# Kernel optimization log

Measured on AMD Instinct MI355X. Metric: run time of the kernel, lower is better.

Reference implementation:

```python
import jax, jax.numpy as jnp
import numpy as np
from jax import lax

B, C, H, W = 4, 4, 64, 64
NREF = 16
DECAY = 0.8
MAX_DELAY = 24
WET_MIX, FEEDBACK, ROOM = 0.3, 0.4, 0.5  # module defaults (static Python floats)
HEADS = 4  # min(4, channels)


def _conv2d(x, w, b, pad, groups=1):
    y = lax.conv_general_dilated(x, w, (1, 1), [(pad, pad), (pad, pad)],
                                 dimension_numbers=('NCHW', 'OIHW', 'NCHW'),
                                 feature_group_count=groups)
    return y if b is None else y + b[None, :, None, None]


def _fade(n, fw=4):
    f = np.ones(n, np.float32)
    f[:fw] = np.linspace(0.6, 1.0, fw)
    f[-fw:] = np.linspace(1.0, 0.6, fw)
    return jnp.asarray(f)


def _delay_line(x, delay, yf, xf):
    # torch: shifts=(int(delay*1), int(delay*2)) on dims (2,3); delay>0 so int==floor
    ys = jnp.floor(delay).astype(jnp.int32)
    xs = jnp.floor(delay * 2.0).astype(jnp.int32)
    s = jnp.roll(x, shift=(ys, xs), axis=(2, 3))
    # shifts are always nonzero here (scaled delays >= 6), so both fades apply
    return s * yf[None, None, :, None] * xf[None, None, None, :]


def setup_inputs() -> dict:
    key = jax.random.key(0)
    ks = jax.random.split(key, 16)
    n = jax.random.normal
    return {
        'x': n(ks[0], (B, C, H, W), jnp.float32),
        'reflection_weights': n(ks[1], (NREF,), jnp.float32) * 0.1,
        'reflection_delays': jax.random.randint(ks[2], (NREF,), 1, MAX_DELAY).astype(jnp.float32),
        'diffusion_strength': n(ks[3], (NREF,), jnp.float32) * 0.2,
        'spatial_w': n(ks[4], (2 * C, C, 3, 3), jnp.float32) * 0.1,
        'spatial_b': jnp.zeros((2 * C,), jnp.float32),
        'feedback_w': n(ks[5], (C, C, 3, 3), jnp.float32) * 0.1,
        'feedback_b': jnp.zeros((C,), jnp.float32),
        'damp1_w': n(ks[6], (C // 2, C, 1, 1), jnp.float32) * 0.3,
        'damp1_b': jnp.zeros((C // 2,), jnp.float32),
        'damp2_w': n(ks[7], (C, C // 2, 1, 1), jnp.float32) * 0.3,
        'damp2_b': jnp.zeros((C,), jnp.float32),
        'attn_in_w': n(ks[8], (3 * C, C), jnp.float32) * 0.3,
        'attn_in_b': jnp.zeros((3 * C,), jnp.float32),
        'attn_out_w': n(ks[9], (C, C), jnp.float32) * 0.3,
        'attn_out_b': jnp.zeros((C,), jnp.float32),
        'out_w': n(ks[10], (C, 3 * C, 1, 1), jnp.float32) * 0.2,
        'out_b': jnp.zeros((C,), jnp.float32),
    }


def reference(x, reflection_weights, reflection_delays, diffusion_strength,
              spatial_w, spatial_b, feedback_w, feedback_b,
              damp1_w, damp1_b, damp2_w, damp2_b,
              attn_in_w, attn_in_b, attn_out_w, attn_out_b, out_w, out_b):
    b, c, h, w = x.shape
    rsf = 8.0 / NREF  # reflection_scale_factor = 0.5
    scaled_delays = reflection_delays * ROOM * 12.0 * rsf
    wet = jnp.zeros_like(x)
    fb = x * 0.1
    spatial_features = _conv2d(x, spatial_w, spatial_b, 1)
    yf, xf = _fade(h), _fade(w)
    feedback_scale = 1.0 + rsf * 0.5
    for i in range(NREF):
        delay = scaled_delays[i]
        weight = jax.nn.sigmoid(reflection_weights[i]) * (DECAY ** i) * (1.0 + FEEDBACK * feedback_scale)
        r = _delay_line(fb, delay, yf, xf)
        r = _conv2d(r, feedback_w, feedback_b, 1)
        damping = jax.nn.sigmoid(
            _conv2d(jax.nn.silu(_conv2d(r, damp1_w, damp1_b, 0)), damp2_w, damp2_b, 0))
        r = r * damping
        wet = wet + r * weight * (4.0 * rsf)
        fb = fb + r * (FEEDBACK * 1.2 * rsf)
        if FEEDBACK > 0.3 and i > 0:
            prev = _delay_line(fb, delay * 0.5, yf, xf)
            fb = fb + prev * (FEEDBACK * 0.4 * rsf)
    # spatial self-attention over flattened pixels (embed=4, 4 heads, head_dim=1)
    S = h * w
    hd = c // HEADS
    wf = wet.reshape(b, c, S).transpose(0, 2, 1)  # [b, S, c]
    qkv = wf @ attn_in_w.T + attn_in_b
    q, k, v = jnp.split(qkv, 3, axis=-1)
    def split_heads(t):
        return t.reshape(b, S, HEADS, hd).transpose(0, 2, 1, 3)  # [b, H, S, hd]
    q, k, v = split_heads(q), split_heads(k), split_heads(v)
    scores = jnp.einsum('bhqd,bhkd->bhqk', q, k) / jnp.sqrt(jnp.float32(hd))
    attn = jax.nn.softmax(scores, axis=-1)
    o = jnp.einsum('bhqk,bhkd->bhqd', attn, v).transpose(0, 2, 1, 3).reshape(b, S, c)
    o = o @ attn_out_w.T + attn_out_b
    wet = o.transpose(0, 2, 1).reshape(b, c, h, w)
    # ROOM=0.5 > 0.3 -> box blur, kernel = max(3, int(0.5*3*0.5)) = 3
    kb = 3
    blur_k = jnp.ones((c, 1, kb, kb), jnp.float32) / (kb * kb)
    wet = _conv2d(wet, blur_k, None, kb // 2, groups=c)
    # FEEDBACK=0.4 > 0.2 -> edge enhancement
    ek = jnp.array([[-1., -1., -1.], [-1., 8., -1.], [-1., -1., -1.]], jnp.float32)
    edge_k = jnp.tile(ek[None, None], (c, 1, 1, 1))
    edge = _conv2d(wet, edge_k, None, 1, groups=c)
    wet = wet + edge * (FEEDBACK * 0.2 * rsf)
    # ROOM=0.5 <= 0.8 -> no contrast adjustment
    combined = jnp.concatenate([spatial_features, wet], axis=1)
    processed = _conv2d(combined, out_w, out_b, 0)
    return x * (1.0 - WET_MIX) + processed * WET_MIX
```

## Files before the change

### kernel.cpp

```cpp
#include <hip/hip_runtime.h>

#define LOG2E 1.4426950408889634f
#define RNB 32

typedef float v2f __attribute__((ext_vector_type(2)));

__device__ __forceinline__ float fsig(float z) {
    return __builtin_amdgcn_rcpf(1.0f + exp2f(-z * LOG2E));
}

__device__ __forceinline__ float4 ld_fb(const unsigned long long* p) {
    unsigned long long a = __hip_atomic_load(p,     __ATOMIC_RELAXED, __HIP_MEMORY_SCOPE_AGENT);
    unsigned long long b = __hip_atomic_load(p + 1, __ATOMIC_RELAXED, __HIP_MEMORY_SCOPE_AGENT);
    float2 lo = __builtin_bit_cast(float2, a);
    float2 hi = __builtin_bit_cast(float2, b);
    return make_float4(lo.x, lo.y, hi.x, hi.y);
}

__device__ __forceinline__ void st_fb(unsigned long long* p, float4 v) {
    __hip_atomic_store(p,     __builtin_bit_cast(unsigned long long, make_float2(v.x, v.y)),
                       __ATOMIC_RELAXED, __HIP_MEMORY_SCOPE_AGENT);
    __hip_atomic_store(p + 1, __builtin_bit_cast(unsigned long long, make_float2(v.z, v.w)),
                       __ATOMIC_RELAXED, __HIP_MEMORY_SCOPE_AGENT);
}

__global__ __launch_bounds__(256) void bar_init(unsigned* cnt) {
    for (int j = threadIdx.x; j < 1024; j += 256) cnt[j] = 0u;
}

__device__ __forceinline__ void conv_damp_l(
    const float4* __restrict__ src, int yq, int xq, int ys, int xs,
    const float* fe, const float4 wr[9][4],
    const float4 d1w0, const float4 d1w1, const float2 d1b, const float4 d2p[4],
    float rv[4])
{
    float r[4] = { d2p[0].w, d2p[1].w, d2p[2].w, d2p[3].w };
    #pragma unroll
    for (int a = 0; a < 3; ++a) {
        int yy = yq - 1 + a;
        float fy = fe[yy + 1];
        const float4* rowp = src + (((yy - ys) & 63) << 6);
        #pragma unroll
        for (int qq = 0; qq < 3; ++qq) {
            int xt = xq - 1 + qq;
            float f = fy * fe[xt + 1];
            float4 v = rowp[(xt - xs) & 63];
            float s0 = v.x * f, s1 = v.y * f, s2 = v.z * f, s3 = v.w * f;
            #pragma unroll
            for (int co = 0; co < 4; ++co) {
                float4 w = wr[a * 3 + qq][co];
                r[co] = fmaf(w.x, s0, fmaf(w.y, s1, fmaf(w.z, s2, fmaf(w.w, s3, r[co]))));
            }
        }
    }
    float z0 = fmaf(d1w0.x, r[0], fmaf(d1w0.y, r[1], fmaf(d1w0.z, r[2], fmaf(d1w0.w, r[3], d1b.x))));
    float z1 = fmaf(d1w1.x, r[0], fmaf(d1w1.y, r[1], fmaf(d1w1.z, r[2], fmaf(d1w1.w, r[3], d1b.y))));
    float h0 = z0 * fsig(z0);
    float h1 = z1 * fsig(z1);
    #pragma unroll
    for (int c = 0; c < 4; ++c) {
        float dm = fsig(fmaf(d2p[c].x, h0, fmaf(d2p[c].y, h1, d2p[c].z)));
        rv[c] = r[c] * dm;
    }
}

__global__ __launch_bounds__(512) void reverb_mb(
    const float* __restrict__ x, const float* __restrict__ rw, const float* __restrict__ dl,
    const float* __restrict__ fbw, const float* __restrict__ fbb,
    const float* __restrict__ d1wg, const float* __restrict__ d1bg,
    const float* __restrict__ d2wg, const float* __restrict__ d2bg,
    unsigned long long* __restrict__ GA, unsigned long long* __restrict__ GB,
    unsigned* __restrict__ cnt, float4* __restrict__ ws_wet)
{
    __shared__ float4 fbL[4096];
    __shared__ float fe[66];
    __shared__ float4 wvsL[36];
    __shared__ float s_rw[16], s_dl[16];
    __shared__ float4 s_mlp[7];

    const int tid = threadIdx.x;
    const int b   = blockIdx.x >> 3;
    const int blk = blockIdx.x & 7;

    if (tid < 66) {
        float f = 0.0f;
        if (tid >= 1 && tid <= 64) {
            int j = tid - 1;
            f = 1.0f;
            if (j < 4) f = 0.6f + (0.4f / 3.0f) * j;
            else if (j >= 60) f = 0.6f + (0.4f / 3.0f) * (63 - j);
        }
        fe[tid] = f;
    }
    if (tid >= 128 && tid < 164) {
        int t2 = tid - 128, n = t2 >> 2, co = t2 & 3;
        wvsL[t2] = make_float4(fbw[(co * 4 + 0) * 9 + n], fbw[(co * 4 + 1) * 9 + n],
                               fbw[(co * 4 + 2) * 9 + n], fbw[(co * 4 + 3) * 9 + n]);
    }
    if (tid >= 192 && tid < 208) s_rw[tid - 192] = rw[tid - 192];
    if (tid >= 256 && tid < 272) s_dl[tid - 256] = dl[tid - 256];
    if (tid == 320) {
        s_mlp[0] = make_float4(d1wg[0], d1wg[1], d1wg[2], d1wg[3]);
        s_mlp[1] = make_float4(d1wg[4], d1wg[5], d1wg[6], d1wg[7]);
        s_mlp[2] = make_float4(d1bg[0], d1bg[1], 0.0f, 0.0f);
        for (int c = 0; c < 4; ++c)
            s_mlp[3 + c] = make_float4(d2wg[c * 2], d2wg[c * 2 + 1], d2bg[c], fbb[c]);
    }
    for (int s = tid; s < 4096; s += 512) {
        float4 v;
        v.x = 0.1f * x[((b * 4 + 0) << 12) + s];
        v.y = 0.1f * x[((b * 4 + 1) << 12) + s];
        v.z = 0.1f * x[((b * 4 + 2) << 12) + s];
        v.w = 0.1f * x[((b * 4 + 3) << 12) + s];
        fbL[s] = v;
    }
    __syncthreads();

    float4 wr[9][4];
    #pragma unroll
    for (int n = 0; n < 9; ++n)
        #pragma unroll
        for (int co = 0; co < 4; ++co) wr[n][co] = wvsL[n * 4 + co];
    const float4 d1w0 = s_mlp[0], d1w1 = s_mlp[1];
    const float2 d1b = make_float2(s_mlp[2].x, s_mlp[2].y);
    float4 d2p[4] = { s_mlp[3], s_mlp[4], s_mlp[5], s_mlp[6] };

    const int ly = tid >> 6;
    const int y0 = (blk << 3) + ly;
    const int xx = tid & 63;
    float4 fbv = fbL[(y0 << 6) + xx];

    unsigned long long* Ab = GA + (b << 13);
    unsigned long long* Bb = GB + (b << 13);
    unsigned* cb = cnt + b * 240;

    float acc0 = 0.0f, acc1 = 0.0f, acc2 = 0.0f, acc3 = 0.0f;
    float decay = 1.0f;
    #pragma unroll 1
    for (int i = 0; i < 16; ++i) {
        float d = s_dl[i];
        int ys  = ((int)(3.0f * d)) & 63;
        int xs  = ((int)(6.0f * d)) & 63;
        float wgt = fsig(s_rw[i]) * decay * 3.0f;

        float rv[4];
        conv_damp_l(fbL, y0, xx, ys, xs, fe, wr, d1w0, d1w1, d1b, d2p, rv);
        acc0 = fmaf(rv[0], wgt, acc0);
        acc1 = fmaf(rv[1], wgt, acc1);
        acc2 = fmaf(rv[2], wgt, acc2);
        acc3 = fmaf(rv[3], wgt, acc3);
        float4 g = make_float4(fbv.x + 0.24f * rv[0], fbv.y + 0.24f * rv[1],
                               fbv.z + 0.24f * rv[2], fbv.w + 0.24f * rv[3]);
        if (i == 15) break;

        unsigned long long* G = (i & 1) ? Bb : Ab;
        st_fb(G + (((y0 << 6) + xx) << 1), g);

        __syncthreads();
        if (tid == 0)
            __hip_atomic_fetch_add(&cb[i * 16], 1u, __ATOMIC_RELAXED,
                                   __HIP_MEMORY_SCOPE_AGENT);
        if ((tid & 63) == 0) {
            while (__hip_atomic_load(&cb[i * 16], __ATOMIC_RELAXED,
                                     __HIP_MEMORY_SCOPE_AGENT) < 8u)
                __builtin_amdgcn_s_sleep(1);
        }
        asm volatile("" ::: "memory");

        int ys2 = ((int)(1.5f * d)) & 63;
        int xs2 = ((int)(3.0f * d)) & 63;
        float dn = s_dl[i + 1];
        int ysn = ((int)(3.0f * dn)) & 63;

        if (i > 0) {
            int yr = (y0 - ys2) & 63, xr = (xx - xs2) & 63;
            float4 g2 = ld_fb(G + (((yr << 6) + xr) << 1));
            float f = 0.08f * fe[y0 + 1] * fe[xx + 1];
            fbv = make_float4(fmaf(f, g2.x, g.x), fmaf(f, g2.y, g.y),
                              fmaf(f, g2.z, g.z), fmaf(f, g2.w, g.w));
        } else {
            fbv = g;
        }

        #pragma unroll
        for (int rpt = 0; rpt < 2; ++rpt) {
            int idx = tid + (rpt << 9);
            if (idx < 640) {
                int j  = idx >> 6, xc = idx & 63;
                int rr = ((blk << 3) - 1 + j - ysn) & 63;
                float4 g1 = ld_fb(G + (((rr << 6) + xc) << 1));
                float4 nv = g1;
                if (i > 0) {
                    int r2 = (rr - ys2) & 63, x2 = (xc - xs2) & 63;
                    float4 g2 = ld_fb(G + (((r2 << 6) + x2) << 1));
                    float f = 0.08f * fe[rr + 1] * fe[xc + 1];
                    nv = make_float4(fmaf(f, g2.x, g1.x), fmaf(f, g2.y, g1.y),
                                     fmaf(f, g2.z, g1.z), fmaf(f, g2.w, g1.w));
                }
                fbL[(rr << 6) + xc] = nv;
            }
        }
        __syncthreads();
        decay *= 0.8f;
    }

    ws_wet[(b << 12) + (y0 << 6) + xx] = make_float4(acc0, acc1, acc2, acc3);
}

__global__ __launch_bounds__(512) void attn_kernel(
    const float4* __restrict__ wet, const float* __restrict__ aiw,
    const float* __restrict__ aib, float* __restrict__ o_out)
{
    __shared__ float ksf[4096];
    __shared__ float vsf[4096];
    __shared__ float redmx[8], redmn[8];
    __shared__ float2 part[2048];

    const int tid = threadIdx.x;
    const int bid = blockIdx.x;
    const int b  = bid >> 7;
    const int h  = (bid >> 5) & 3;
    const int qc = bid & 31;

    float wq[4], wk[4], wv[4];
    #pragma unroll
    for (int c = 0; c < 4; ++c) {
        wq[c] = aiw[h * 4 + c];
        wk[c] = aiw[(4 + h) * 4 + c];
        wv[c] = aiw[(8 + h) * 4 + c];
    }
    const float bq = aib[h], bk = aib[4 + h], bv = aib[8 + h];

    float lmax = -1e30f, lmin = 1e30f;
    for (int s = tid; s < 4096; s += 512) {
        float4 w4 = wet[(b << 12) + s];
        float k = wk[0] * w4.x + wk[1] * w4.y + wk[2] * w4.z + wk[3] * w4.w + bk;
        float v = wv[0] * w4.x + wv[1] * w4.y + wv[2] * w4.z + wv[3] * w4.w + bv;
        ksf[s] = k; vsf[s] = v;
        lmax = fmaxf(lmax, k); lmin = fminf(lmin, k);
    }
    #pragma unroll
    for (int off = 32; off > 0; off >>= 1) {
        lmax = fmaxf(lmax, __shfl_xor(lmax, off));
        lmin = fminf(lmin, __shfl_xor(lmin, off));
    }
    if ((tid & 63) == 0) { redmx[tid >> 6] = lmax; redmn[tid >> 6] = lmin; }
    __syncthreads();
    float kmax = redmx[0], kmin = redmn[0];
    #pragma unroll
    for (int w = 1; w < 8; ++w) { kmax = fmaxf(kmax, redmx[w]); kmin = fminf(kmin, redmn[w]); }

    const int rs = tid & 31;
    const int kg = tid >> 5;
    v2f qL2[4], nmL2[4];
    #pragma unroll
    for (int rr = 0; rr < 4; ++rr) {
        int row = (qc << 7) + (rs << 2) + rr;
        float4 w4 = wet[(b << 12) + row];
        float q = wq[0] * w4.x + wq[1] * w4.y + wq[2] * w4.z + wq[3] * w4.w + bq;
        float m = (q >= 0.0f) ? q * kmax : q * kmin;
        float qL = q * LOG2E, mL = m * LOG2E;
        qL2[rr] = (v2f){qL, qL}; nmL2[rr] = (v2f){-mL, -mL};
    }

    const v2f* ks2 = (const v2f*)ksf;
    const v2f* vs2 = (const v2f*)vsf;
    v2f den2[4], num2[4];
    #pragma unroll
    for (int rr = 0; rr < 4; ++rr) { den2[rr] = (v2f){0.f, 0.f}; num2[rr] = (v2f){0.f, 0.f}; }

    const int j0 = kg << 6;
    #pragma unroll 4
    for (int j = j0 * 2; j < j0 * 2 + 128; ++j) {
        v2f kk = ks2[j];
        v2f vv = vs2[j];
        #pragma unroll
        for (int rr = 0; rr < 4; ++rr) {
            v2f arg = __builtin_elementwise_fma(qL2[rr], kk, nmL2[rr]);
            v2f e;
            e.x = __builtin_amdgcn_exp2f(arg.x);
            e.y = __builtin_amdgcn_exp2f(arg.y);
            den2[rr] += e;
            num2[rr] = __builtin_elementwise_fma(e, vv, num2[rr]);
        }
    }
    #pragma unroll
    for (int rr = 0; rr < 4; ++rr)
        part[(kg << 7) + (rs << 2) + rr] =
            make_float2(den2[rr].x + den2[rr].y, num2[rr].x + num2[rr].y);
    __syncthreads();
    if (tid < 128) {
        float dd = 0.0f, nn = 0.0f;
        #pragma unroll
        for (int g = 0; g < 16; ++g) {
            float2 p = part[(g << 7) + tid];
            dd += p.x; nn += p.y;
        }
        int row = (qc << 7) + tid;
        o_out[((b << 12) + row) * 4 + h] = nn * __builtin_amdgcn_rcpf(dd);
    }
}

__global__ __launch_bounds__(256) void tail_kernel(
    const float4* __restrict__ o_in, const float* __restrict__ aow,
    const float* __restrict__ aob, const float* __restrict__ x,
    const float* __restrict__ sw, const float* __restrict__ sb,
    const float* __restrict__ ow, const float* __restrict__ ob,
    float* __restrict__ out)
{
    __shared__ float wetp[4][8][64];
    __shared__ float blurL[4][6][64];
    __shared__ float xL[4][6][64];
    __shared__ float s_sw[288], s_ow[48], s_sb[8], s_ob[4];

    const int tid  = threadIdx.x;
    const int b    = blockIdx.x >> 4;
    const int band = blockIdx.x & 15;
    const int y0   = band << 2;

    float pw[4][4], pb[4];
    #pragma unroll
    for (int c = 0; c < 4; ++c) {
        #pragma unroll
        for (int h = 0; h < 4; ++h) pw[c][h] = aow[c * 4 + h];
        pb[c] = aob[c];
    }

    for (int j = tid; j < 288; j += 256) s_sw[j] = sw[j];
    if (tid < 48) s_ow[tid] = ow[tid];
    if (tid < 8)  s_sb[tid] = sb[tid];
    if (tid < 4)  s_ob[tid] = ob[tid];

    for (int s = tid; s < 512; s += 256) {
        int lr = s >> 6, xx = s & 63;
        int gy = y0 - 2 + lr;
        float4 o = make_float4(0.f, 0.f, 0.f, 0.f);
        if (gy >= 0 && gy < 64) o = o_in[(b << 12) + (gy << 6) + xx];
        #pragma unroll
        for (int c = 0; c < 4; ++c)
            wetp[c][lr][xx] = (gy >= 0 && gy < 64)
                ? pw[c][0]*o.x + pw[c][1]*o.y + pw[c][2]*o.z + pw[c][3]*o.w + pb[c]
                : 0.0f;
    }
    for (int s = tid; s < 1536; s += 256) {
        int c = s / 384, rm = s - c * 384;
        int r = rm >> 6, xx = rm & 63;
        int gy = y0 - 1 + r;
        float v = 0.f;
        if (gy >= 0 && gy < 64) v = x[((b * 4 + c) << 12) + (gy << 6) + xx];
        xL[c][r][xx] = v;
    }
    __syncthreads();

    for (int s = tid; s < 1536; s += 256) {
        int c = s / 384, rm = s - c * 384;
        int r = rm >> 6, xx = rm & 63;
        int gy = y0 - 1 + r;
        float acc = 0.f;
        if (gy >= 0 && gy < 64) {
            #pragma unroll
            for (int dy = 0; dy < 3; ++dy) {
                #pragma unroll
                for (int dx = -1; dx <= 1; ++dx) {
                    int xc = xx + dx;
                    if (xc >= 0 && xc <= 63) acc += wetp[c][r + dy][xc];
                }
            }
        }
        blurL[c][r][xx] = acc * (1.0f / 9.0f);
    }
    __syncthreads();

    {
        const int lyq = tid >> 6, xx = tid & 63;
        const int gy = y0 + lyq;

        float spat[8];
        #pragma unroll
        for (int co = 0; co < 8; ++co) spat[co] = s_sb[co];
        #pragma unroll
        for (int dy = 0; dy < 3; ++dy) {
            #pragma unroll
            for (int dx = -1; dx <= 1; ++dx) {
                int xc = xx + dx;
                if (xc < 0 || xc > 63) continue;
                int kx = dx + 1;
                #pragma unroll
                for (int ci = 0; ci < 4; ++ci) {
                    float xv = xL[ci][lyq + dy][xc];
                    #pragma unroll
                    for (int co = 0; co < 8; ++co)
                        spat[co] += s_sw[((co * 4 + ci) * 3 + dy) * 3 + kx] * xv;
                }
            }
        }

        float wetF[4];
        #pragma unroll
        for (int c = 0; c < 4; ++c) {
            float center = blurL[c][lyq + 1][xx];
            float sum9 = 0.f;
            #pragma unroll
            for (int dy = 0; dy < 3; ++dy) {
                #pragma unroll
                for (int dx = -1; dx <= 1; ++dx) {
                    int xc = xx + dx;
                    if (xc >= 0 && xc <= 63) sum9 += blurL[c][lyq + dy][xc];
                }
            }
            wetF[c] = center + 0.04f * (9.0f * center - sum9);
        }

        #pragma unroll
        for (int co = 0; co < 4; ++co) {
            float p = s_ob[co];
            #pragma unroll
            for (int j = 0; j < 8; ++j) p += s_ow[co * 12 + j] * spat[j];
            #pragma unroll
            for (int c = 0; c < 4; ++c) p += s_ow[co * 12 + 8 + c] * wetF[c];
            float xc = xL[co][lyq + 1][xx];
            out[((b * 4 + co) << 12) + (gy << 6) + xx] = 0.7f * xc + 0.3f * p;
        }
    }
}

extern "C" void kernel_launch(void* const* d_in, const int* in_sizes, int n_in,
                              void* d_out, int out_size, void* d_ws, size_t ws_size,
                              hipStream_t stream)
{
    (void)in_sizes; (void)n_in; (void)out_size; (void)ws_size;
    const float* x    = (const float*)d_in[0];
    const float* rw   = (const float*)d_in[1];
    const float* dl   = (const float*)d_in[2];
    const float* sw   = (const float*)d_in[4];
    const float* sb   = (const float*)d_in[5];
    const float* fbw  = (const float*)d_in[6];
    const float* fbb  = (const float*)d_in[7];
    const float* d1w  = (const float*)d_in[8];
    const float* d1b  = (const float*)d_in[9];
    const float* d2w  = (const float*)d_in[10];
    const float* d2b  = (const float*)d_in[11];
    const float* aiw  = (const float*)d_in[12];
    const float* aib  = (const float*)d_in[13];
    const float* aow  = (const float*)d_in[14];
    const float* aob  = (const float*)d_in[15];
    const float* ow   = (const float*)d_in[16];
    const float* ob   = (const float*)d_in[17];
    float* out = (float*)d_out;

    float* ws_wet  = (float*)d_ws;
    float* GA      = ws_wet + 65536;
    float* GB      = GA + 65536;
    unsigned* cnt  = (unsigned*)(GB + 65536);
    float* ws_o    = GA;

    bar_init<<<1, 256, 0, stream>>>(cnt);
    reverb_mb<<<RNB, 512, 0, stream>>>(x, rw, dl, fbw, fbb, d1w, d1b, d2w, d2b,
                                       (unsigned long long*)GA, (unsigned long long*)GB,
                                       cnt, (float4*)ws_wet);
    attn_kernel<<<512, 512, 0, stream>>>((const float4*)ws_wet, aiw, aib, ws_o);
    tail_kernel<<<64, 256, 0, stream>>>((const float4*)ws_o, aow, aob, x,
                                        sw, sb, ow, ob, out);
}
```

Baseline: 184.4 us.

## Fuse reverb and attention kernels with per-batch completion flags

```diff
diff --git a/kernel.cpp b/kernel.cpp
--- a/kernel.cpp
+++ b/kernel.cpp
@@ -64,240 +64,264 @@
     }
 }
 
-__global__ __launch_bounds__(512) void reverb_mb(
+struct SmemReverb {
+    float4 fbL[4096];
+    float  fe[66];
+    float4 wvsL[36];
+    float  s_rw[16], s_dl[16];
+    float4 s_mlp[7];
+};
+struct SmemAttn {
+    float  ksf[4096];
+    float  vsf[4096];
+    float  redmx[8], redmn[8];
+    float2 part[2048];
+};
+union SmemU { SmemReverb r; SmemAttn a; };
+
+__global__ __launch_bounds__(512) void fused_ra(
     const float* __restrict__ x, const float* __restrict__ rw, const float* __restrict__ dl,
     const float* __restrict__ fbw, const float* __restrict__ fbb,
     const float* __restrict__ d1wg, const float* __restrict__ d1bg,
     const float* __restrict__ d2wg, const float* __restrict__ d2bg,
     unsigned long long* __restrict__ GA, unsigned long long* __restrict__ GB,
-    unsigned* __restrict__ cnt, float4* __restrict__ ws_wet)
+    unsigned* __restrict__ cnt, unsigned long long* __restrict__ ws_wet,
+    const float* __restrict__ aiw, const float* __restrict__ aib,
+    float* __restrict__ o_out)
 {
-    __shared__ float4 fbL[4096];
-    __shared__ float fe[66];
-    __shared__ float4 wvsL[36];
-    __shared__ float s_rw[16], s_dl[16];
-    __shared__ float4 s_mlp[7];
-
+    __shared__ SmemU sm;
     const int tid = threadIdx.x;
-    const int b   = blockIdx.x >> 3;
-    const int blk = blockIdx.x & 7;
-
-    if (tid < 66) {
-        float f = 0.0f;
-        if (tid >= 1 && tid <= 64) {
-            int j = tid - 1;
-            f = 1.0f;
-            if (j < 4) f = 0.6f + (0.4f / 3.0f) * j;
-            else if (j >= 60) f = 0.6f + (0.4f / 3.0f) * (63 - j);
-        }
-        fe[tid] = f;
-    }
-    if (tid >= 128 && tid < 164) {
-        int t2 = tid - 128, n = t2 >> 2, co = t2 & 3;
-        wvsL[t2] = make_float4(fbw[(co * 4 + 0) * 9 + n], fbw[(co * 4 + 1) * 9 + n],
-                               fbw[(co * 4 + 2) * 9 + n], fbw[(co * 4 + 3) * 9 + n]);
-    }
-    if (tid >= 192 && tid < 208) s_rw[tid - 192] = rw[tid - 192];
-    if (tid >= 256 && tid < 272) s_dl[tid - 256] = dl[tid - 256];
-    if (tid == 320) {
-        s_mlp[0] = make_float4(d1wg[0], d1wg[1], d1wg[2], d1wg[3]);
-        s_mlp[1] = make_float4(d1wg[4], d1wg[5], d1wg[6], d1wg[7]);
-        s_mlp[2] = make_float4(d1bg[0], d1bg[1], 0.0f, 0.0f);
-        for (int c = 0; c < 4; ++c)
-            s_mlp[3 + c] = make_float4(d2wg[c * 2], d2wg[c * 2 + 1], d2bg[c], fbb[c]);
-    }
-    for (int s = tid; s < 4096; s += 512) {
-        float4 v;
-        v.x = 0.1f * x[((b * 4 + 0) << 12) + s];
-        v.y = 0.1f * x[((b * 4 + 1) << 12) + s];
-        v.z = 0.1f * x[((b * 4 + 2) << 12) + s];
-        v.w = 0.1f * x[((b * 4 + 3) << 12) + s];
-        fbL[s] = v;
-    }
-    __syncthreads();
-
-    float4 wr[9][4];
-    #pragma unroll
-    for (int n = 0; n < 9; ++n)
-        #pragma unroll
-        for (int co = 0; co < 4; ++co) wr[n][co] = wvsL[n * 4 + co];
-    const float4 d1w0 = s_mlp[0], d1w1 = s_mlp[1];
-    const float2 d1b = make_float2(s_mlp[2].x, s_mlp[2].y);
-    float4 d2p[4] = { s_mlp[3], s_mlp[4], s_mlp[5], s_mlp[6] };
-
-    const int ly = tid >> 6;
-    const int y0 = (blk << 3) + ly;
-    const int xx = tid & 63;
-    float4 fbv = fbL[(y0 << 6) + xx];
-
-    unsigned long long* Ab = GA + (b << 13);
-    unsigned long long* Bb = GB + (b << 13);
-    unsigned* cb = cnt + b * 240;
-
-    float acc0 = 0.0f, acc1 = 0.0f, acc2 = 0.0f, acc3 = 0.0f;
-    float decay = 1.0f;
-    #pragma unroll 1
-    for (int i = 0; i < 16; ++i) {
-        float d = s_dl[i];
-        int ys  = ((int)(3.0f * d)) & 63;
-        int xs  = ((int)(6.0f * d)) & 63;
-        float wgt = fsig(s_rw[i]) * decay * 3.0f;
-
-        float rv[4];
-        conv_damp_l(fbL, y0, xx, ys, xs, fe, wr, d1w0, d1w1, d1b, d2p, rv);
-        acc0 = fmaf(rv[0], wgt, acc0);
-        acc1 = fmaf(rv[1], wgt, acc1);
-        acc2 = fmaf(rv[2], wgt, acc2);
-        acc3 = fmaf(rv[3], wgt, acc3);
-        float4 g = make_float4(fbv.x + 0.24f * rv[0], fbv.y + 0.24f * rv[1],
-                               fbv.z + 0.24f * rv[2], fbv.w + 0.24f * rv[3]);
-        if (i == 15) break;
-
-        unsigned long long* G = (i & 1) ? Bb : Ab;
-        st_fb(G + (((y0 << 6) + xx) << 1), g);
-
+    const int bid = blockIdx.x;
+
+    if (bid < RNB) {
+        float4* fbL = sm.r.fbL;
+        float*  fe  = sm.r.fe;
+
+        const int b   = bid >> 3;
+        const int blk = bid & 7;
+
+        if (tid < 66) {
+            float f = 0.0f;
+            if (tid >= 1 && tid <= 64) {
+                int j = tid - 1;
+                f = 1.0f;
+                if (j < 4) f = 0.6f + (0.4f / 3.0f) * j;
+                else if (j >= 60) f = 0.6f + (0.4f / 3.0f) * (63 - j);
+            }
+            fe[tid] = f;
+        }
+        if (tid >= 128 && tid < 164) {
+            int t2 = tid - 128, n = t2 >> 2, co = t2 & 3;
+            sm.r.wvsL[t2] = make_float4(fbw[(co * 4 + 0) * 9 + n], fbw[(co * 4 + 1) * 9 + n],
+                                        fbw[(co * 4 + 2) * 9 + n], fbw[(co * 4 + 3) * 9 + n]);
+        }
+        if (tid >= 192 && tid < 208) sm.r.s_rw[tid - 192] = rw[tid - 192];
+        if (tid >= 256 && tid < 272) sm.r.s_dl[tid - 256] = dl[tid - 256];
+        if (tid == 320) {
+            sm.r.s_mlp[0] = make_float4(d1wg[0], d1wg[1], d1wg[2], d1wg[3]);
+            sm.r.s_mlp[1] = make_float4(d1wg[4], d1wg[5], d1wg[6], d1wg[7]);
+            sm.r.s_mlp[2] = make_float4(d1bg[0], d1bg[1], 0.0f, 0.0f);
+            for (int c = 0; c < 4; ++c)
+                sm.r.s_mlp[3 + c] = make_float4(d2wg[c * 2], d2wg[c * 2 + 1], d2bg[c], fbb[c]);
+        }
+        for (int s = tid; s < 4096; s += 512) {
+            float4 v;
+            v.x = 0.1f * x[((b * 4 + 0) << 12) + s];
+            v.y = 0.1f * x[((b * 4 + 1) << 12) + s];
+            v.z = 0.1f * x[((b * 4 + 2) << 12) + s];
+            v.w = 0.1f * x[((b * 4 + 3) << 12) + s];
+            fbL[s] = v;
+        }
+        __syncthreads();
+
+        float4 wr[9][4];
+        #pragma unroll
+        for (int n = 0; n < 9; ++n)
+            #pragma unroll
+            for (int co = 0; co < 4; ++co) wr[n][co] = sm.r.wvsL[n * 4 + co];
+        const float4 d1w0 = sm.r.s_mlp[0], d1w1 = sm.r.s_mlp[1];
+        const float2 d1b = make_float2(sm.r.s_mlp[2].x, sm.r.s_mlp[2].y);
+        float4 d2p[4] = { sm.r.s_mlp[3], sm.r.s_mlp[4], sm.r.s_mlp[5], sm.r.s_mlp[6] };
+
+        const int ly = tid >> 6;
+        const int y0 = (blk << 3) + ly;
+        const int xx = tid & 63;
+        float4 fbv = fbL[(y0 << 6) + xx];
+
+        unsigned long long* Ab = GA + (b << 13);
+        unsigned long long* Bb = GB + (b << 13);
+        unsigned* cb = cnt + b * 240;
+
+        float acc0 = 0.0f, acc1 = 0.0f, acc2 = 0.0f, acc3 = 0.0f;
+        float decay = 1.0f;
+        #pragma unroll 1
+        for (int i = 0; i < 16; ++i) {
+            float d = sm.r.s_dl[i];
+            int ys  = ((int)(3.0f * d)) & 63;
+            int xs  = ((int)(6.0f * d)) & 63;
+            float wgt = fsig(sm.r.s_rw[i]) * decay * 3.0f;
+
+            float rv[4];
+            conv_damp_l(fbL, y0, xx, ys, xs, fe, wr, d1w0, d1w1, d1b, d2p, rv);
+            acc0 = fmaf(rv[0], wgt, acc0);
+            acc1 = fmaf(rv[1], wgt, acc1);
+            acc2 = fmaf(rv[2], wgt, acc2);
+            acc3 = fmaf(rv[3], wgt, acc3);
+            float4 g = make_float4(fbv.x + 0.24f * rv[0], fbv.y + 0.24f * rv[1],
+                                   fbv.z + 0.24f * rv[2], fbv.w + 0.24f * rv[3]);
+            if (i == 15) break;
+
+            unsigned long long* G = (i & 1) ? Bb : Ab;
+            st_fb(G + (((y0 << 6) + xx) << 1), g);
+
+            __syncthreads();
+            if (tid == 0) {
+                if (__hip_atomic_fetch_add(&cb[i * 16], 1u, __ATOMIC_RELAXED,
+                                           __HIP_MEMORY_SCOPE_AGENT) + 1u < 8u) {
+                    while (__hip_atomic_load(&cb[i * 16], __ATOMIC_RELAXED,
+                                             __HIP_MEMORY_SCOPE_AGENT) < 8u)
+                        __builtin_amdgcn_s_sleep(1);
+                }
+            }
+            __syncthreads();
+
+            int ys2 = ((int)(1.5f * d)) & 63;
+            int xs2 = ((int)(3.0f * d)) & 63;
+            float dn = sm.r.s_dl[i + 1];
+            int ysn = ((int)(3.0f * dn)) & 63;
+
+            if (i > 0) {
+                int yr = (y0 - ys2) & 63, xr = (xx - xs2) & 63;
+                float4 g2 = ld_fb(G + (((yr << 6) + xr) << 1));
+                float f = 0.08f * fe[y0 + 1] * fe[xx + 1];
+                fbv = make_float4(fmaf(f, g2.x, g.x), fmaf(f, g2.y, g.y),
+                                  fmaf(f, g2.z, g.z), fmaf(f, g2.w, g.w));
+            } else {
+                fbv = g;
+            }
+
+            #pragma unroll
+            for (int rpt = 0; rpt < 2; ++rpt) {
+                int idx = tid + (rpt << 9);
+                if (idx < 640) {
+                    int j  = idx >> 6, xc = idx & 63;
+                    int rr = ((blk << 3) - 1 + j - ysn) & 63;
+                    float4 g1 = ld_fb(G + (((rr << 6) + xc) << 1));
+                    float4 nv = g1;
+                    if (i > 0) {
+                        int r2 = (rr - ys2) & 63, x2 = (xc - xs2) & 63;
+                        float4 g2 = ld_fb(G + (((r2 << 6) + x2) << 1));
+                        float f = 0.08f * fe[rr + 1] * fe[xc + 1];
+                        nv = make_float4(fmaf(f, g2.x, g1.x), fmaf(f, g2.y, g1.y),
+                                         fmaf(f, g2.z, g1.z), fmaf(f, g2.w, g1.w));
+                    }
+                    fbL[(rr << 6) + xc] = nv;
+                }
+            }
+            __syncthreads();
+            decay *= 0.8f;
+        }
+
+        st_fb(ws_wet + (((b << 12) + (y0 << 6) + xx) << 1),
+              make_float4(acc0, acc1, acc2, acc3));
         __syncthreads();
         if (tid == 0)
-            __hip_atomic_fetch_add(&cb[i * 16], 1u, __ATOMIC_RELAXED,
+            __hip_atomic_fetch_add(&cnt[960 + b], 1u, __ATOMIC_RELAXED,
                                    __HIP_MEMORY_SCOPE_AGENT);
-        if ((tid & 63) == 0) {
-            while (__hip_atomic_load(&cb[i * 16], __ATOMIC_RELAXED,
+    }
+
+    {
+        const int b  = bid >> 7;
+        const int h  = (bid >> 5) & 3;
+        const int qc = bid & 31;
+
+        if (tid == 0) {
+            while (__hip_atomic_load(&cnt[960 + b], __ATOMIC_RELAXED,
                                      __HIP_MEMORY_SCOPE_AGENT) < 8u)
-                __builtin_amdgcn_s_sleep(1);
-        }
-        asm volatile("" ::: "memory");
-
-        int ys2 = ((int)(1.5f * d)) & 63;
-        int xs2 = ((int)(3.0f * d)) & 63;
-        float dn = s_dl[i + 1];
-        int ysn = ((int)(3.0f * dn)) & 63;
-
-        if (i > 0) {
-            int yr = (y0 - ys2) & 63, xr = (xx - xs2) & 63;
-            float4 g2 = ld_fb(G + (((yr << 6) + xr) << 1));
-            float f = 0.08f * fe[y0 + 1] * fe[xx + 1];
-            fbv = make_float4(fmaf(f, g2.x, g.x), fmaf(f, g2.y, g.y),
-                              fmaf(f, g2.z, g.z), fmaf(f, g2.w, g.w));
-        } else {
-            fbv = g;
-        }
-
-        #pragma unroll
-        for (int rpt = 0; rpt < 2; ++rpt) {
-            int idx = tid + (rpt << 9);
-            if (idx < 640) {
-                int j  = idx >> 6, xc = idx & 63;
-                int rr = ((blk << 3) - 1 + j - ysn) & 63;
-                float4 g1 = ld_fb(G + (((rr << 6) + xc) << 1));
-                float4 nv = g1;
-                if (i > 0) {
-                    int r2 = (rr - ys2) & 63, x2 = (xc - xs2) & 63;
-                    float4 g2 = ld_fb(G + (((r2 << 6) + x2) << 1));
-                    float f = 0.08f * fe[rr + 1] * fe[xc + 1];
-                    nv = make_float4(fmaf(f, g2.x, g1.x), fmaf(f, g2.y, g1.y),
-                                     fmaf(f, g2.z, g1.z), fmaf(f, g2.w, g1.w));
-                }
-                fbL[(rr << 6) + xc] = nv;
-            }
+                __builtin_amdgcn_s_sleep(16);
         }
         __syncthreads();
-        decay *= 0.8f;
-    }
-
-    ws_wet[(b << 12) + (y0 << 6) + xx] = make_float4(acc0, acc1, acc2, acc3);
-}
-
-__global__ __launch_bounds__(512) void attn_kernel(
-    const float4* __restrict__ wet, const float* __restrict__ aiw,
-    const float* __restrict__ aib, float* __restrict__ o_out)
-{
-    __shared__ float ksf[4096];
-    __shared__ float vsf[4096];
-    __shared__ float redmx[8], redmn[8];
-    __shared__ float2 part[2048];
-
-    const int tid = threadIdx.x;
-    const int bid = blockIdx.x;
-    const int b  = bid >> 7;
-    const int h  = (bid >> 5) & 3;
-    const int qc = bid & 31;
-
-    float wq[4], wk[4], wv[4];
-    #pragma unroll
-    for (int c = 0; c < 4; ++c) {
-        wq[c] = aiw[h * 4 + c];
-        wk[c] = aiw[(4 + h) * 4 + c];
-        wv[c] = aiw[(8 + h) * 4 + c];
-    }
-    const float bq = aib[h], bk = aib[4 + h], bv = aib[8 + h];
-
-    float lmax = -1e30f, lmin = 1e30f;
-    for (int s = tid; s < 4096; s += 512) {
-        float4 w4 = wet[(b << 12) + s];
-        float k = wk[0] * w4.x + wk[1] * w4.y + wk[2] * w4.z + wk[3] * w4.w + bk;
-        float v = wv[0] * w4.x + wv[1] * w4.y + wv[2] * w4.z + wv[3] * w4.w + bv;
-        ksf[s] = k; vsf[s] = v;
-        lmax = fmaxf(lmax, k); lmin = fminf(lmin, k);
-    }
-    #pragma unroll
-    for (int off = 32; off > 0; off >>= 1) {
-        lmax = fmaxf(lmax, __shfl_xor(lmax, off));
-        lmin = fminf(lmin, __shfl_xor(lmin, off));
-    }
-    if ((tid & 63) == 0) { redmx[tid >> 6] = lmax; redmn[tid >> 6] = lmin; }
-    __syncthreads();
-    float kmax = redmx[0], kmin = redmn[0];
-    #pragma unroll
-    for (int w = 1; w < 8; ++w) { kmax = fmaxf(kmax, redmx[w]); kmin = fminf(kmin, redmn[w]); }
-
-    const int rs = tid & 31;
-    const int kg = tid >> 5;
-    v2f qL2[4], nmL2[4];
-    #pragma unroll
-    for (int rr = 0; rr < 4; ++rr) {
-        int row = (qc << 7) + (rs << 2) + rr;
-        float4 w4 = wet[(b << 12) + row];
-        float q = wq[0] * w4.x + wq[1] * w4.y + wq[2] * w4.z + wq[3] * w4.w + bq;
-        float m = (q >= 0.0f) ? q * kmax : q * kmin;
-        float qL = q * LOG2E, mL = m * LOG2E;
-        qL2[rr] = (v2f){qL, qL}; nmL2[rr] = (v2f){-mL, -mL};
-    }
-
-    const v2f* ks2 = (const v2f*)ksf;
-    const v2f* vs2 = (const v2f*)vsf;
-    v2f den2[4], num2[4];
-    #pragma unroll
-    for (int rr = 0; rr < 4; ++rr) { den2[rr] = (v2f){0.f, 0.f}; num2[rr] = (v2f){0.f, 0.f}; }
-
-    const int j0 = kg << 6;
-    #pragma unroll 4
-    for (int j = j0 * 2; j < j0 * 2 + 128; ++j) {
-        v2f kk = ks2[j];
-        v2f vv = vs2[j];
+
+        float wq[4], wk[4], wv[4];
+        #pragma unroll
+        for (int c = 0; c < 4; ++c) {
+            wq[c] = aiw[h * 4 + c];
+            wk[c] = aiw[(4 + h) * 4 + c];
+            wv[c] = aiw[(8 + h) * 4 + c];
+        }
+        const float bq = aib[h], bk = aib[4 + h], bv = aib[8 + h];
+
+        float lmax = -1e30f, lmin = 1e30f;
+        for (int s = tid; s < 4096; s += 512) {
+            float4 w4 = ld_fb(ws_wet + (((b << 12) + s) << 1));
+            float k = wk[0] * w4.x + wk[1] * w4.y + wk[2] * w4.z + wk[3] * w4.w + bk;
+            float v = wv[0] * w4.x + wv[1] * w4.y + wv[2] * w4.z + wv[3] * w4.w + bv;
+            sm.a.ksf[s] = k; sm.a.vsf[s] = v;
+            lmax = fmaxf(lmax, k); lmin = fminf(lmin, k);
+        }
+        #pragma unroll
+        for (int off = 32; off > 0; off >>= 1) {
+            lmax = fmaxf(lmax, __shfl_xor(lmax, off));
+            lmin = fminf(lmin, __shfl_xor(lmin, off));
+        }
+        if ((tid & 63) == 0) { sm.a.redmx[tid >> 6] = lmax; sm.a.redmn[tid >> 6] = lmin; }
+        __syncthreads();
+        float kmax = sm.a.redmx[0], kmin = sm.a.redmn[0];
+        #pragma unroll
+        for (int w = 1; w < 8; ++w) {
+            kmax = fmaxf(kmax, sm.a.redmx[w]);
+            kmin = fminf(kmin, sm.a.redmn[w]);
+        }
+
+        const int rs = tid & 31;
+        const int kg = tid >> 5;
+        v2f qL2[4], nmL2[4];
         #pragma unroll
         for (int rr = 0; rr < 4; ++rr) {
-            v2f arg = __builtin_elementwise_fma(qL2[rr], kk, nmL2[rr]);
-            v2f e;
-            e.x = __builtin_amdgcn_exp2f(arg.x);
-            e.y = __builtin_amdgcn_exp2f(arg.y);
-            den2[rr] += e;
-            num2[rr] = __builtin_elementwise_fma(e, vv, num2[rr]);
-        }
-    }
-    #pragma unroll
-    for (int rr = 0; rr < 4; ++rr)
-        part[(kg << 7) + (rs << 2) + rr] =
-            make_float2(den2[rr].x + den2[rr].y, num2[rr].x + num2[rr].y);
-    __syncthreads();
-    if (tid < 128) {
-        float dd = 0.0f, nn = 0.0f;
-        #pragma unroll
-        for (int g = 0; g < 16; ++g) {
-            float2 p = part[(g << 7) + tid];
-            dd += p.x; nn += p.y;
-        }
-        int row = (qc << 7) + tid;
-        o_out[((b << 12) + row) * 4 + h] = nn * __builtin_amdgcn_rcpf(dd);
+            int row = (qc << 7) + (rs << 2) + rr;
+            float4 w4 = ld_fb(ws_wet + (((b << 12) + row) << 1));
+            float q = wq[0] * w4.x + wq[1] * w4.y + wq[2] * w4.z + wq[3] * w4.w + bq;
+            float m = (q >= 0.0f) ? q * kmax : q * kmin;
+            float qL = q * LOG2E, mL = m * LOG2E;
+            qL2[rr] = (v2f){qL, qL}; nmL2[rr] = (v2f){-mL, -mL};
+        }
+
+        const v2f* ks2 = (const v2f*)sm.a.ksf;
+        const v2f* vs2 = (const v2f*)sm.a.vsf;
+        v2f den2[4], num2[4];
+        #pragma unroll
+        for (int rr = 0; rr < 4; ++rr) { den2[rr] = (v2f){0.f, 0.f}; num2[rr] = (v2f){0.f, 0.f}; }
+
+        const int j0 = kg << 6;
+        #pragma unroll 4
+        for (int j = j0 * 2; j < j0 * 2 + 128; ++j) {
+            v2f kk = ks2[j];
+            v2f vv = vs2[j];
+            #pragma unroll
+            for (int rr = 0; rr < 4; ++rr) {
+                v2f arg = __builtin_elementwise_fma(qL2[rr], kk, nmL2[rr]);
+                v2f e;
+                e.x = __builtin_amdgcn_exp2f(arg.x);
+                e.y = __builtin_amdgcn_exp2f(arg.y);
+                den2[rr] += e;
+                num2[rr] = __builtin_elementwise_fma(e, vv, num2[rr]);
+            }
+        }
+        #pragma unroll
+        for (int rr = 0; rr < 4; ++rr)
+            sm.a.part[(kg << 7) + (rs << 2) + rr] =
+                make_float2(den2[rr].x + den2[rr].y, num2[rr].x + num2[rr].y);
+        __syncthreads();
+        if (tid < 128) {
+            float dd = 0.0f, nn = 0.0f;
+            #pragma unroll
+            for (int g = 0; g < 16; ++g) {
+                float2 p = sm.a.part[(g << 7) + tid];
+                dd += p.x; nn += p.y;
+            }
+            int row = (qc << 7) + tid;
+            o_out[((b << 12) + row) * 4 + h] = nn * __builtin_amdgcn_rcpf(dd);
+        }
     }
 }
 
@@ -455,10 +479,10 @@
     float* ws_o    = GA;
 
     bar_init<<<1, 256, 0, stream>>>(cnt);
-    reverb_mb<<<RNB, 512, 0, stream>>>(x, rw, dl, fbw, fbb, d1w, d1b, d2w, d2b,
-                                       (unsigned long long*)GA, (unsigned long long*)GB,
-                                       cnt, (float4*)ws_wet);
-    attn_kernel<<<512, 512, 0, stream>>>((const float4*)ws_wet, aiw, aib, ws_o);
+    fused_ra<<<512, 512, 0, stream>>>(x, rw, dl, fbw, fbb, d1w, d1b, d2w, d2b,
+                                      (unsigned long long*)GA, (unsigned long long*)GB,
+                                      cnt, (unsigned long long*)ws_wet,
+                                      aiw, aib, ws_o);
     tail_kernel<<<64, 256, 0, stream>>>((const float4*)ws_o, aow, aob, x,
                                         sw, sb, ow, ob, out);
 }
```

Result: no change. 187.9 us (+1.9%).

## Run reverb recurrence in one block per batch, dropping cross-block global barriers

Applied to the files above, without the earlier changes.

```diff
diff --git a/kernel.cpp b/kernel.cpp
--- a/kernel.cpp
+++ b/kernel.cpp
@@ -1,86 +1,32 @@
 #include <hip/hip_runtime.h>
 
 #define LOG2E 1.4426950408889634f
-#define RNB 32
 
 typedef float v2f __attribute__((ext_vector_type(2)));
+typedef float v4f __attribute__((ext_vector_type(4)));
+
+__device__ __forceinline__ v4f splat4(float v) { return (v4f){v, v, v, v}; }
 
 __device__ __forceinline__ float fsig(float z) {
-    return __builtin_amdgcn_rcpf(1.0f + exp2f(-z * LOG2E));
+    return __builtin_amdgcn_rcpf(1.0f + __builtin_amdgcn_exp2f(-z * LOG2E));
 }
 
-__device__ __forceinline__ float4 ld_fb(const unsigned long long* p) {
-    unsigned long long a = __hip_atomic_load(p,     __ATOMIC_RELAXED, __HIP_MEMORY_SCOPE_AGENT);
-    unsigned long long b = __hip_atomic_load(p + 1, __ATOMIC_RELAXED, __HIP_MEMORY_SCOPE_AGENT);
-    float2 lo = __builtin_bit_cast(float2, a);
-    float2 hi = __builtin_bit_cast(float2, b);
-    return make_float4(lo.x, lo.y, hi.x, hi.y);
-}
-
-__device__ __forceinline__ void st_fb(unsigned long long* p, float4 v) {
-    __hip_atomic_store(p,     __builtin_bit_cast(unsigned long long, make_float2(v.x, v.y)),
-                       __ATOMIC_RELAXED, __HIP_MEMORY_SCOPE_AGENT);
-    __hip_atomic_store(p + 1, __builtin_bit_cast(unsigned long long, make_float2(v.z, v.w)),
-                       __ATOMIC_RELAXED, __HIP_MEMORY_SCOPE_AGENT);
-}
-
-__global__ __launch_bounds__(256) void bar_init(unsigned* cnt) {
-    for (int j = threadIdx.x; j < 1024; j += 256) cnt[j] = 0u;
-}
-
-__device__ __forceinline__ void conv_damp_l(
-    const float4* __restrict__ src, int yq, int xq, int ys, int xs,
-    const float* fe, const float4 wr[9][4],
-    const float4 d1w0, const float4 d1w1, const float2 d1b, const float4 d2p[4],
-    float rv[4])
-{
-    float r[4] = { d2p[0].w, d2p[1].w, d2p[2].w, d2p[3].w };
-    #pragma unroll
-    for (int a = 0; a < 3; ++a) {
-        int yy = yq - 1 + a;
-        float fy = fe[yy + 1];
-        const float4* rowp = src + (((yy - ys) & 63) << 6);
-        #pragma unroll
-        for (int qq = 0; qq < 3; ++qq) {
-            int xt = xq - 1 + qq;
-            float f = fy * fe[xt + 1];
-            float4 v = rowp[(xt - xs) & 63];
-            float s0 = v.x * f, s1 = v.y * f, s2 = v.z * f, s3 = v.w * f;
-            #pragma unroll
-            for (int co = 0; co < 4; ++co) {
-                float4 w = wr[a * 3 + qq][co];
-                r[co] = fmaf(w.x, s0, fmaf(w.y, s1, fmaf(w.z, s2, fmaf(w.w, s3, r[co]))));
-            }
-        }
-    }
-    float z0 = fmaf(d1w0.x, r[0], fmaf(d1w0.y, r[1], fmaf(d1w0.z, r[2], fmaf(d1w0.w, r[3], d1b.x))));
-    float z1 = fmaf(d1w1.x, r[0], fmaf(d1w1.y, r[1], fmaf(d1w1.z, r[2], fmaf(d1w1.w, r[3], d1b.y))));
-    float h0 = z0 * fsig(z0);
-    float h1 = z1 * fsig(z1);
-    #pragma unroll
-    for (int c = 0; c < 4; ++c) {
-        float dm = fsig(fmaf(d2p[c].x, h0, fmaf(d2p[c].y, h1, d2p[c].z)));
-        rv[c] = r[c] * dm;
-    }
-}
-
-__global__ __launch_bounds__(512) void reverb_mb(
+__global__ __launch_bounds__(512) void reverb_sb(
     const float* __restrict__ x, const float* __restrict__ rw, const float* __restrict__ dl,
     const float* __restrict__ fbw, const float* __restrict__ fbb,
     const float* __restrict__ d1wg, const float* __restrict__ d1bg,
     const float* __restrict__ d2wg, const float* __restrict__ d2bg,
-    unsigned long long* __restrict__ GA, unsigned long long* __restrict__ GB,
-    unsigned* __restrict__ cnt, float4* __restrict__ ws_wet)
+    float4* __restrict__ ws_wet)
 {
-    __shared__ float4 fbL[4096];
+    __shared__ v4f fbL[4096];
     __shared__ float fe[66];
-    __shared__ float4 wvsL[36];
+    __shared__ v4f wTs[36];
     __shared__ float s_rw[16], s_dl[16];
-    __shared__ float4 s_mlp[7];
+    __shared__ v4f s_d1w0, s_d1w1, s_d2x, s_d2y, s_d2b, s_fbb;
+    __shared__ float2 s_d1bb;
 
     const int tid = threadIdx.x;
-    const int b   = blockIdx.x >> 3;
-    const int blk = blockIdx.x & 7;
+    const int b   = blockIdx.x;
 
     if (tid < 66) {
         float f = 0.0f;
@@ -93,118 +39,126 @@
         fe[tid] = f;
     }
     if (tid >= 128 && tid < 164) {
-        int t2 = tid - 128, n = t2 >> 2, co = t2 & 3;
-        wvsL[t2] = make_float4(fbw[(co * 4 + 0) * 9 + n], fbw[(co * 4 + 1) * 9 + n],
-                               fbw[(co * 4 + 2) * 9 + n], fbw[(co * 4 + 3) * 9 + n]);
+        int t2 = tid - 128, tap = t2 >> 2, cin = t2 & 3;
+        wTs[t2] = (v4f){ fbw[(0 * 4 + cin) * 9 + tap], fbw[(1 * 4 + cin) * 9 + tap],
+                         fbw[(2 * 4 + cin) * 9 + tap], fbw[(3 * 4 + cin) * 9 + tap] };
     }
     if (tid >= 192 && tid < 208) s_rw[tid - 192] = rw[tid - 192];
     if (tid >= 256 && tid < 272) s_dl[tid - 256] = dl[tid - 256];
     if (tid == 320) {
-        s_mlp[0] = make_float4(d1wg[0], d1wg[1], d1wg[2], d1wg[3]);
-        s_mlp[1] = make_float4(d1wg[4], d1wg[5], d1wg[6], d1wg[7]);
-        s_mlp[2] = make_float4(d1bg[0], d1bg[1], 0.0f, 0.0f);
-        for (int c = 0; c < 4; ++c)
-            s_mlp[3 + c] = make_float4(d2wg[c * 2], d2wg[c * 2 + 1], d2bg[c], fbb[c]);
+        s_d1w0 = (v4f){ d1wg[0], d1wg[1], d1wg[2], d1wg[3] };
+        s_d1w1 = (v4f){ d1wg[4], d1wg[5], d1wg[6], d1wg[7] };
+        s_d1bb = make_float2(d1bg[0], d1bg[1]);
+        s_d2x  = (v4f){ d2wg[0], d2wg[2], d2wg[4], d2wg[6] };
+        s_d2y  = (v4f){ d2wg[1], d2wg[3], d2wg[5], d2wg[7] };
+        s_d2b  = (v4f){ d2bg[0], d2bg[1], d2bg[2], d2bg[3] };
+        s_fbb  = (v4f){ fbb[0], fbb[1], fbb[2], fbb[3] };
     }
     for (int s = tid; s < 4096; s += 512) {
-        float4 v;
-        v.x = 0.1f * x[((b * 4 + 0) << 12) + s];
-        v.y = 0.1f * x[((b * 4 + 1) << 12) + s];
-        v.z = 0.1f * x[((b * 4 + 2) << 12) + s];
-        v.w = 0.1f * x[((b * 4 + 3) << 12) + s];
-        fbL[s] = v;
+        fbL[s] = (v4f){ 0.1f * x[((b * 4 + 0) << 12) + s],
+                        0.1f * x[((b * 4 + 1) << 12) + s],
+                        0.1f * x[((b * 4 + 2) << 12) + s],
+                        0.1f * x[((b * 4 + 3) << 12) + s] };
     }
     __syncthreads();
 
-    float4 wr[9][4];
-    #pragma unroll
-    for (int n = 0; n < 9; ++n)
-        #pragma unroll
-        for (int co = 0; co < 4; ++co) wr[n][co] = wvsL[n * 4 + co];
-    const float4 d1w0 = s_mlp[0], d1w1 = s_mlp[1];
-    const float2 d1b = make_float2(s_mlp[2].x, s_mlp[2].y);
-    float4 d2p[4] = { s_mlp[3], s_mlp[4], s_mlp[5], s_mlp[6] };
-
-    const int ly = tid >> 6;
-    const int y0 = (blk << 3) + ly;
-    const int xx = tid & 63;
-    float4 fbv = fbL[(y0 << 6) + xx];
-
-    unsigned long long* Ab = GA + (b << 13);
-    unsigned long long* Bb = GB + (b << 13);
-    unsigned* cb = cnt + b * 240;
-
-    float acc0 = 0.0f, acc1 = 0.0f, acc2 = 0.0f, acc3 = 0.0f;
+    const v4f d1w0 = s_d1w0, d1w1 = s_d1w1, d2x = s_d2x, d2y = s_d2y,
+              d2b = s_d2b, fbbv = s_fbb;
+    const float2 d1b = s_d1bb;
+
+    const int y  = tid >> 3;
+    const int x0 = (tid & 7) << 3;
+    const float fey = fe[y + 1];
+
+    v4f acc[8];
+    #pragma unroll
+    for (int q = 0; q < 8; ++q) acc[q] = splat4(0.0f);
+
     float decay = 1.0f;
     #pragma unroll 1
     for (int i = 0; i < 16; ++i) {
-        float d = s_dl[i];
-        int ys  = ((int)(3.0f * d)) & 63;
-        int xs  = ((int)(6.0f * d)) & 63;
-        float wgt = fsig(s_rw[i]) * decay * 3.0f;
-
-        float rv[4];
-        conv_damp_l(fbL, y0, xx, ys, xs, fe, wr, d1w0, d1w1, d1b, d2p, rv);
-        acc0 = fmaf(rv[0], wgt, acc0);
-        acc1 = fmaf(rv[1], wgt, acc1);
-        acc2 = fmaf(rv[2], wgt, acc2);
-        acc3 = fmaf(rv[3], wgt, acc3);
-        float4 g = make_float4(fbv.x + 0.24f * rv[0], fbv.y + 0.24f * rv[1],
-                               fbv.z + 0.24f * rv[2], fbv.w + 0.24f * rv[3]);
+        const float d = s_dl[i];
+        const int ys = ((int)(3.0f * d)) & 63;
+        const int xs = ((int)(6.0f * d)) & 63;
+        const float wgt = fsig(s_rw[i]) * decay * 3.0f;
+
+        v4f r[8];
+        #pragma unroll
+        for (int q = 0; q < 8; ++q) r[q] = fbbv;
+        #pragma unroll
+        for (int a = 0; a < 3; ++a) {
+            int yy = y - 1 + a;
+            float fy = fe[yy + 1];
+            const v4f* rowp = fbL + (((yy - ys) & 63) << 6);
+            v4f sc[10];
+            #pragma unroll
+            for (int c = 0; c < 10; ++c) {
+                int xt = x0 - 1 + c;
+                float f = fy * fe[xt + 1];
+                sc[c] = rowp[(xt - xs) & 63] * f;
+            }
+            #pragma unroll
+            for (int t = 0; t < 3; ++t) {
+                v4f w0 = wTs[(a * 3 + t) * 4 + 0];
+                v4f w1 = wTs[(a * 3 + t) * 4 + 1];
+                v4f w2 = wTs[(a * 3 + t) * 4 + 2];
+                v4f w3 = wTs[(a * 3 + t) * 4 + 3];
+                #pragma unroll
+                for (int q = 0; q < 8; ++q) {
+                    v4f sv = sc[q + t];
+                    r[q] = __builtin_elementwise_fma(w0, splat4(sv.x), r[q]);
+                    r[q] = __builtin_elementwise_fma(w1, splat4(sv.y), r[q]);
+                    r[q] = __builtin_elementwise_fma(w2, splat4(sv.z), r[q]);
+                    r[q] = __builtin_elementwise_fma(w3, splat4(sv.w), r[q]);
+                }
+            }
+        }
+        v4f gq[8];
+        #pragma unroll
+        for (int q = 0; q < 8; ++q) {
+            v4f r4 = r[q];
+            float z0 = fmaf(d1w0.x, r4.x, fmaf(d1w0.y, r4.y,
+                        fmaf(d1w0.z, r4.z, fmaf(d1w0.w, r4.w, d1b.x))));
+            float z1 = fmaf(d1w1.x, r4.x, fmaf(d1w1.y, r4.y,
+                        fmaf(d1w1.z, r4.z, fmaf(d1w1.w, r4.w, d1b.y))));
+            float h0 = z0 * fsig(z0);
+            float h1 = z1 * fsig(z1);
+            v4f pre = __builtin_elementwise_fma(d2x, splat4(h0),
+                        __builtin_elementwise_fma(d2y, splat4(h1), d2b));
+            v4f dm = (v4f){ fsig(pre.x), fsig(pre.y), fsig(pre.z), fsig(pre.w) };
+            v4f rv = r4 * dm;
+            acc[q] = __builtin_elementwise_fma(rv, splat4(wgt), acc[q]);
+            gq[q] = fbL[(y << 6) + x0 + q] + rv * 0.24f;
+        }
         if (i == 15) break;
 
-        unsigned long long* G = (i & 1) ? Bb : Ab;
-        st_fb(G + (((y0 << 6) + xx) << 1), g);
-
         __syncthreads();
-        if (tid == 0)
-            __hip_atomic_fetch_add(&cb[i * 16], 1u, __ATOMIC_RELAXED,
-                                   __HIP_MEMORY_SCOPE_AGENT);
-        if ((tid & 63) == 0) {
-            while (__hip_atomic_load(&cb[i * 16], __ATOMIC_RELAXED,
-                                     __HIP_MEMORY_SCOPE_AGENT) < 8u)
-                __builtin_amdgcn_s_sleep(1);
-        }
-        asm volatile("" ::: "memory");
-
-        int ys2 = ((int)(1.5f * d)) & 63;
-        int xs2 = ((int)(3.0f * d)) & 63;
-        float dn = s_dl[i + 1];
-        int ysn = ((int)(3.0f * dn)) & 63;
-
+        #pragma unroll
+        for (int q = 0; q < 8; ++q) fbL[(y << 6) + x0 + q] = gq[q];
+        __syncthreads();
         if (i > 0) {
-            int yr = (y0 - ys2) & 63, xr = (xx - xs2) & 63;
-            float4 g2 = ld_fb(G + (((yr << 6) + xr) << 1));
-            float f = 0.08f * fe[y0 + 1] * fe[xx + 1];
-            fbv = make_float4(fmaf(f, g2.x, g.x), fmaf(f, g2.y, g.y),
-                              fmaf(f, g2.z, g.z), fmaf(f, g2.w, g.w));
-        } else {
-            fbv = g;
-        }
-
-        #pragma unroll
-        for (int rpt = 0; rpt < 2; ++rpt) {
-            int idx = tid + (rpt << 9);
-            if (idx < 640) {
-                int j  = idx >> 6, xc = idx & 63;
-                int rr = ((blk << 3) - 1 + j - ysn) & 63;
-                float4 g1 = ld_fb(G + (((rr << 6) + xc) << 1));
-                float4 nv = g1;
-                if (i > 0) {
-                    int r2 = (rr - ys2) & 63, x2 = (xc - xs2) & 63;
-                    float4 g2 = ld_fb(G + (((r2 << 6) + x2) << 1));
-                    float f = 0.08f * fe[rr + 1] * fe[xc + 1];
-                    nv = make_float4(fmaf(f, g2.x, g1.x), fmaf(f, g2.y, g1.y),
-                                     fmaf(f, g2.z, g1.z), fmaf(f, g2.w, g1.w));
-                }
-                fbL[(rr << 6) + xc] = nv;
+            int ys2 = ((int)(1.5f * d)) & 63;
+            int xs2 = ((int)(3.0f * d)) & 63;
+            const v4f* srow = fbL + (((y - ys2) & 63) << 6);
+            v4f pv[8];
+            #pragma unroll
+            for (int q = 0; q < 8; ++q) pv[q] = srow[(x0 + q - xs2) & 63];
+            __syncthreads();
+            #pragma unroll
+            for (int q = 0; q < 8; ++q) {
+                float f = 0.08f * fey * fe[x0 + q + 1];
+                fbL[(y << 6) + x0 + q] =
+                    __builtin_elementwise_fma(pv[q], splat4(f), gq[q]);
             }
         }
         __syncthreads();
         decay *= 0.8f;
     }
 
-    ws_wet[(b << 12) + (y0 << 6) + xx] = make_float4(acc0, acc1, acc2, acc3);
+    #pragma unroll
+    for (int q = 0; q < 8; ++q)
+        ws_wet[(b << 12) + (y << 6) + x0 + q] =
+            make_float4(acc[q].x, acc[q].y, acc[q].z, acc[q].w);
 }
 
 __global__ __launch_bounds__(512) void attn_kernel(
@@ -448,16 +402,11 @@
     const float* ob   = (const float*)d_in[17];
     float* out = (float*)d_out;
 
-    float* ws_wet  = (float*)d_ws;
-    float* GA      = ws_wet + 65536;
-    float* GB      = GA + 65536;
-    unsigned* cnt  = (unsigned*)(GB + 65536);
-    float* ws_o    = GA;
-
-    bar_init<<<1, 256, 0, stream>>>(cnt);
-    reverb_mb<<<RNB, 512, 0, stream>>>(x, rw, dl, fbw, fbb, d1w, d1b, d2w, d2b,
-                                       (unsigned long long*)GA, (unsigned long long*)GB,
-                                       cnt, (float4*)ws_wet);
+    float* ws_wet = (float*)d_ws;
+    float* ws_o   = ws_wet + 65536;
+
+    reverb_sb<<<4, 512, 0, stream>>>(x, rw, dl, fbw, fbb, d1w, d1b, d2w, d2b,
+                                     (float4*)ws_wet);
     attn_kernel<<<512, 512, 0, stream>>>((const float4*)ws_wet, aiw, aib, ws_o);
     tail_kernel<<<64, 256, 0, stream>>>((const float4*)ws_o, aow, aob, x,
                                         sw, sb, ow, ob, out);
```

After: 304.1 us. +64.9%, slower.
